# Optimization experiments

Measured on AMD Instinct MI355X. Metric: run time of the kernel, lower is better.

Reference implementation:

```python
import jax, jax.numpy as jnp
import numpy as np

B, MUL = 512, 64
DIMS = {0: 1, 1: 3, 2: 5}
PAIRS = [(0, 0), (0, 1), (0, 2), (1, 1), (1, 2), (2, 2)]  # l2 >= l1 (filter_symmetric)
LS_OUT = (0, 1, 2)


def _triples():
    for l1, l2 in PAIRS:
        for l3 in range(abs(l1 - l2), l1 + l2 + 1):
            if l3 in LS_OUT:
                yield (l1, l2, l3)


def setup_inputs() -> dict:
    key = jax.random.key(0)
    inp = {}
    for l in LS_OUT:
        key, k = jax.random.split(key)
        inp['x%d' % l] = jax.random.normal(k, (B, MUL, DIMS[l]), dtype=jnp.float32)
    for (l1, l2, l3) in _triples():
        key, k = jax.random.split(key)
        inp['w3j_%d_%d_%d' % (l1, l2, l3)] = jax.random.normal(
            k, (DIMS[l1], DIMS[l2], DIMS[l3]), dtype=jnp.float32) * 0.1
    return inp


def _forward(x, w):
    # ls_rule='full', channel_rule='full', filter_symmetric=True
    out = {l3: [] for l3 in LS_OUT}
    for l1, l2 in PAIRS:
        # outer product over channels and m-components: [B, i*j, 2l1+1, 2l2+1]
        op = jnp.einsum('bim,bjn->bijmn', x[l1], x[l2])
        b, i, j, m, n = op.shape
        op = op.reshape(b, i * j, m, n)
        for l3 in range(abs(l1 - l2), l1 + l2 + 1):
            if l3 in LS_OUT:
                # contract with Clebsch-Gordan / w3j coefficients
                out[l3].append(jnp.einsum('mnM,bimn->biM', w[(l1, l2, l3)], op))
    return tuple(jnp.concatenate(out[l3], axis=1) for l3 in LS_OUT)


def reference(x0, x1, x2,
              w3j_0_0_0, w3j_0_1_1, w3j_0_2_2,
              w3j_1_1_0, w3j_1_1_1, w3j_1_1_2,
              w3j_1_2_1, w3j_1_2_2,
              w3j_2_2_0, w3j_2_2_1, w3j_2_2_2):
    x = {0: x0, 1: x1, 2: x2}
    w = {(0, 0, 0): w3j_0_0_0, (0, 1, 1): w3j_0_1_1, (0, 2, 2): w3j_0_2_2,
         (1, 1, 0): w3j_1_1_0, (1, 1, 1): w3j_1_1_1, (1, 1, 2): w3j_1_1_2,
         (1, 2, 1): w3j_1_2_1, (1, 2, 2): w3j_1_2_2,
         (2, 2, 0): w3j_2_2_0, (2, 2, 1): w3j_2_2_1, (2, 2, 2): w3j_2_2_2}
    return _forward(x, w)
```

## Files before the change

kernel.cpp:

```cpp
#include <hip/hip_runtime.h>


#define OUT1_BASE (512 * 12288)
#define OUT2_BASE (OUT1_BASE + 512 * 49152)

template<int D1, int D2, int D3>
__device__ __forceinline__ void do_path(const float* __restrict__ w,
                                        const float* a, const float* bv,
                                        float* __restrict__ op)
{
    float wa[D2 * D3];
#pragma unroll
    for (int k = 0; k < D2 * D3; ++k) wa[k] = 0.f;
#pragma unroll
    for (int m = 0; m < D1; ++m) {
        const float am = a[m];
#pragma unroll
        for (int n = 0; n < D2; ++n)
#pragma unroll
            for (int M = 0; M < D3; ++M)
                wa[n * D3 + M] += w[(m * D2 + n) * D3 + M] * am;
    }

    float o[4 * D3];
#pragma unroll
    for (int k = 0; k < 4 * D3; ++k) o[k] = 0.f;
#pragma unroll
    for (int jj = 0; jj < 4; ++jj)
#pragma unroll
        for (int n = 0; n < D2; ++n) {
            const float bb = bv[jj * D2 + n];
#pragma unroll
            for (int M = 0; M < D3; ++M)
                o[jj * D3 + M] += wa[n * D3 + M] * bb;
        }

#pragma unroll
    for (int q = 0; q < D3; ++q) {
        float4 v;
        v.x = o[4 * q + 0]; v.y = o[4 * q + 1];
        v.z = o[4 * q + 2]; v.w = o[4 * q + 3];
        *(float4*)(op + 4 * q) = v;
    }
}

__global__ __launch_bounds__(256) void tp_kernel(
    const float* __restrict__ x0, const float* __restrict__ x1, const float* __restrict__ x2,
    const float* __restrict__ w000, const float* __restrict__ w011, const float* __restrict__ w022,
    const float* __restrict__ w110, const float* __restrict__ w111, const float* __restrict__ w112,
    const float* __restrict__ w121, const float* __restrict__ w122,
    const float* __restrict__ w220, const float* __restrict__ w221, const float* __restrict__ w222,
    float* __restrict__ out)
{
    const int b   = blockIdx.x >> 2;
    const int seg = blockIdx.x & 3;
    const int t   = threadIdx.x;
    const int c0  = seg * 1024 + t * 4;
    const int i   = c0 >> 6;
    const int j0  = c0 & 63;

    const float a0[1] = { x0[b * 64 + i] };
    float a1[3], a2[5];
#pragma unroll
    for (int m = 0; m < 3; ++m) a1[m] = x1[b * 192 + i * 3 + m];
#pragma unroll
    for (int m = 0; m < 5; ++m) a2[m] = x2[b * 320 + i * 5 + m];

    float b0v[4], b1v[12], b2v[20];
    {
        const float4 v = *(const float4*)(x0 + b * 64 + j0);
        b0v[0] = v.x; b0v[1] = v.y; b0v[2] = v.z; b0v[3] = v.w;
    }
#pragma unroll
    for (int k = 0; k < 3; ++k) {
        const float4 v = *(const float4*)(x1 + b * 192 + j0 * 3 + 4 * k);
        b1v[4 * k + 0] = v.x; b1v[4 * k + 1] = v.y;
        b1v[4 * k + 2] = v.z; b1v[4 * k + 3] = v.w;
    }
#pragma unroll
    for (int k = 0; k < 5; ++k) {
        const float4 v = *(const float4*)(x2 + b * 320 + j0 * 5 + 4 * k);
        b2v[4 * k + 0] = v.x; b2v[4 * k + 1] = v.y;
        b2v[4 * k + 2] = v.z; b2v[4 * k + 3] = v.w;
    }

    float* __restrict__ o0 = out + b * 12288;
    float* __restrict__ o1 = out + OUT1_BASE + b * 49152;
    float* __restrict__ o2 = out + OUT2_BASE + b * 81920;

    do_path<1, 1, 1>(w000, a0, b0v, o0 + 0 * 4096 + c0);

    do_path<1, 3, 3>(w011, a0, b1v, o1 + 0 * 12288 + c0 * 3);

    do_path<1, 5, 5>(w022, a0, b2v, o2 + 0 * 20480 + c0 * 5);

    do_path<3, 3, 1>(w110, a1, b1v, o0 + 1 * 4096 + c0);
    do_path<3, 3, 3>(w111, a1, b1v, o1 + 1 * 12288 + c0 * 3);
    do_path<3, 3, 5>(w112, a1, b1v, o2 + 1 * 20480 + c0 * 5);

    do_path<3, 5, 3>(w121, a1, b2v, o1 + 2 * 12288 + c0 * 3);
    do_path<3, 5, 5>(w122, a1, b2v, o2 + 2 * 20480 + c0 * 5);

    do_path<5, 5, 1>(w220, a2, b2v, o0 + 2 * 4096 + c0);
    do_path<5, 5, 3>(w221, a2, b2v, o1 + 3 * 12288 + c0 * 3);
    do_path<5, 5, 5>(w222, a2, b2v, o2 + 3 * 20480 + c0 * 5);
}

extern "C" void kernel_launch(void* const* d_in, const int* in_sizes, int n_in,
                              void* d_out, int out_size, void* d_ws, size_t ws_size,
                              hipStream_t stream) {
    const float* x0   = (const float*)d_in[0];
    const float* x1   = (const float*)d_in[1];
    const float* x2   = (const float*)d_in[2];
    const float* w000 = (const float*)d_in[3];
    const float* w011 = (const float*)d_in[4];
    const float* w022 = (const float*)d_in[5];
    const float* w110 = (const float*)d_in[6];
    const float* w111 = (const float*)d_in[7];
    const float* w112 = (const float*)d_in[8];
    const float* w121 = (const float*)d_in[9];
    const float* w122 = (const float*)d_in[10];
    const float* w220 = (const float*)d_in[11];
    const float* w221 = (const float*)d_in[12];
    const float* w222 = (const float*)d_in[13];
    float* outp = (float*)d_out;

    dim3 grid(512 * 4);
    dim3 block(256);
    tp_kernel<<<grid, block, 0, stream>>>(x0, x1, x2,
                                          w000, w011, w022, w110, w111, w112,
                                          w121, w122, w220, w221, w222, outp);
}
```

Measured before the change: 358.7 us.

## Stage l=1 and l=2 outputs through shared memory for coalesced stores

After: 320.9 us. -10.5%, faster.

```diff
diff --git a/kernel.cpp b/kernel.cpp
--- a/kernel.cpp
+++ b/kernel.cpp
@@ -5,9 +5,9 @@
 #define OUT2_BASE (OUT1_BASE + 512 * 49152)
 
 template<int D1, int D2, int D3>
-__device__ __forceinline__ void do_path(const float* __restrict__ w,
-                                        const float* a, const float* bv,
-                                        float* __restrict__ op)
+__device__ __forceinline__ void path_compute(const float* __restrict__ w,
+                                             const float* a, const float* bv,
+                                             float* __restrict__ o)
 {
     float wa[D2 * D3];
 #pragma unroll
@@ -21,8 +21,6 @@
             for (int M = 0; M < D3; ++M)
                 wa[n * D3 + M] += w[(m * D2 + n) * D3 + M] * am;
     }
-
-    float o[4 * D3];
 #pragma unroll
     for (int k = 0; k < 4 * D3; ++k) o[k] = 0.f;
 #pragma unroll
@@ -34,14 +32,27 @@
             for (int M = 0; M < D3; ++M)
                 o[jj * D3 + M] += wa[n * D3 + M] * bb;
         }
+}
 
+template<int D3>
+__device__ __forceinline__ void stage(float* __restrict__ s, int dwbase,
+                                      const float* __restrict__ o)
+{
 #pragma unroll
     for (int q = 0; q < D3; ++q) {
         float4 v;
         v.x = o[4 * q + 0]; v.y = o[4 * q + 1];
         v.z = o[4 * q + 2]; v.w = o[4 * q + 3];
-        *(float4*)(op + 4 * q) = v;
+        *(float4*)(s + dwbase + 4 * q) = v;
     }
+}
+
+__device__ __forceinline__ void store_f4(float* __restrict__ p,
+                                         const float* __restrict__ o)
+{
+    float4 v;
+    v.x = o[0]; v.y = o[1]; v.z = o[2]; v.w = o[3];
+    *(float4*)p = v;
 }
 
 __global__ __launch_bounds__(256) void tp_kernel(
@@ -52,6 +63,8 @@
     const float* __restrict__ w220, const float* __restrict__ w221, const float* __restrict__ w222,
     float* __restrict__ out)
 {
+    __shared__ __align__(16) float s_out[8192];
+
     const int b   = blockIdx.x >> 2;
     const int seg = blockIdx.x & 3;
     const int t   = threadIdx.x;
@@ -85,25 +98,52 @@
     }
 
     float* __restrict__ o0 = out + b * 12288;
-    float* __restrict__ o1 = out + OUT1_BASE + b * 49152;
-    float* __restrict__ o2 = out + OUT2_BASE + b * 81920;
+    const int o1base = OUT1_BASE + b * 49152 + seg * 3072;
+    const int o2base = OUT2_BASE + b * 81920 + seg * 5120;
 
-    do_path<1, 1, 1>(w000, a0, b0v, o0 + 0 * 4096 + c0);
+    float o[20];
 
-    do_path<1, 3, 3>(w011, a0, b1v, o1 + 0 * 12288 + c0 * 3);
+    {
+        float oo[4];
+#pragma unroll
+        for (int jj = 0; jj < 4; ++jj) oo[jj] = w000[0] * (a0[0] * b0v[jj]);
+        store_f4(o0 + c0, oo);
+    }
+    path_compute<1, 3, 3>(w011, a0, b1v, o);  stage<3>(s_out, t * 12, o);
+    path_compute<1, 5, 5>(w022, a0, b2v, o);  stage<5>(s_out, 3072 + t * 20, o);
 
-    do_path<1, 5, 5>(w022, a0, b2v, o2 + 0 * 20480 + c0 * 5);
+#pragma unroll
+    for (int r = 0; r < 4; ++r) {
+        __syncthreads();
+#pragma unroll
+        for (int kk = 0; kk < 8; ++kk) {
+            const int fi = kk * 256 + t;
+            float4 v = *(const float4*)(s_out + 4 * fi);
+            int dst;
+            if (fi < 768) dst = o1base + r * 12288 + 4 * fi;
+            else          dst = o2base + r * 20480 + 4 * (fi - 768);
+            *(float4*)(out + dst) = v;
+        }
+        if (r == 3) break;
+        __syncthreads();
 
-    do_path<3, 3, 1>(w110, a1, b1v, o0 + 1 * 4096 + c0);
-    do_path<3, 3, 3>(w111, a1, b1v, o1 + 1 * 12288 + c0 * 3);
-    do_path<3, 3, 5>(w112, a1, b1v, o2 + 1 * 20480 + c0 * 5);
-
-    do_path<3, 5, 3>(w121, a1, b2v, o1 + 2 * 12288 + c0 * 3);
-    do_path<3, 5, 5>(w122, a1, b2v, o2 + 2 * 20480 + c0 * 5);
-
-    do_path<5, 5, 1>(w220, a2, b2v, o0 + 2 * 4096 + c0);
-    do_path<5, 5, 3>(w221, a2, b2v, o1 + 3 * 12288 + c0 * 3);
-    do_path<5, 5, 5>(w222, a2, b2v, o2 + 3 * 20480 + c0 * 5);
+        if (r == 0) {
+            float oo[4];
+            path_compute<3, 3, 1>(w110, a1, b1v, oo);
+            store_f4(o0 + 4096 + c0, oo);
+            path_compute<3, 3, 3>(w111, a1, b1v, o);  stage<3>(s_out, t * 12, o);
+            path_compute<3, 3, 5>(w112, a1, b1v, o);  stage<5>(s_out, 3072 + t * 20, o);
+        } else if (r == 1) {
+            path_compute<3, 5, 3>(w121, a1, b2v, o);  stage<3>(s_out, t * 12, o);
+            path_compute<3, 5, 5>(w122, a1, b2v, o);  stage<5>(s_out, 3072 + t * 20, o);
+        } else {
+            float oo[4];
+            path_compute<5, 5, 1>(w220, a2, b2v, oo);
+            store_f4(o0 + 8192 + c0, oo);
+            path_compute<5, 5, 3>(w221, a2, b2v, o);  stage<3>(s_out, t * 12, o);
+            path_compute<5, 5, 5>(w222, a2, b2v, o);  stage<5>(s_out, 3072 + t * 20, o);
+        }
+    }
 }
 
 extern "C" void kernel_launch(void* const* d_in, const int* in_sizes, int n_in,
```

## Stage l=1/l=2 outputs through per-wave LDS for fully coalesced stores

Applied to the files above, without the earlier changes.

Result: faster. 322.7 us (-10.0%).

```diff
diff --git a/kernel.cpp b/kernel.cpp
--- a/kernel.cpp
+++ b/kernel.cpp
@@ -4,10 +4,15 @@
 #define OUT1_BASE (512 * 12288)
 #define OUT2_BASE (OUT1_BASE + 512 * 49152)
 
+#define LDS_FENCE() do {                                  \
+    asm volatile("s_waitcnt lgkmcnt(0)" ::: "memory");    \
+    __builtin_amdgcn_sched_barrier(0);                    \
+} while (0)
+
 template<int D1, int D2, int D3>
-__device__ __forceinline__ void do_path(const float* __restrict__ w,
-                                        const float* a, const float* bv,
-                                        float* __restrict__ op)
+__device__ __forceinline__ void path_compute(const float* __restrict__ w,
+                                             const float* a, const float* bv,
+                                             float* o)
 {
     float wa[D2 * D3];
 #pragma unroll
@@ -21,8 +26,6 @@
             for (int M = 0; M < D3; ++M)
                 wa[n * D3 + M] += w[(m * D2 + n) * D3 + M] * am;
     }
-
-    float o[4 * D3];
 #pragma unroll
     for (int k = 0; k < 4 * D3; ++k) o[k] = 0.f;
 #pragma unroll
@@ -34,15 +37,42 @@
             for (int M = 0; M < D3; ++M)
                 o[jj * D3 + M] += wa[n * D3 + M] * bb;
         }
+}
 
-#pragma unroll
-    for (int q = 0; q < D3; ++q) {
-        float4 v;
-        v.x = o[4 * q + 0]; v.y = o[4 * q + 1];
-        v.z = o[4 * q + 2]; v.w = o[4 * q + 3];
-        *(float4*)(op + 4 * q) = v;
-    }
-}
+#define STAGE3(optr) do {                                          \
+    _Pragma("unroll")                                              \
+    for (int q = 0; q < 3; ++q) {                                  \
+        float4 v;                                                  \
+        v.x = (optr)[4*q+0]; v.y = (optr)[4*q+1];                  \
+        v.z = (optr)[4*q+2]; v.w = (optr)[4*q+3];                  \
+        *(float4*)(sw + ln * 12 + 4 * q) = v;                      \
+    }                                                              \
+} while (0)
+
+#define STAGE5(optr) do {                                          \
+    _Pragma("unroll")                                              \
+    for (int q = 0; q < 5; ++q) {                                  \
+        float4 v;                                                  \
+        v.x = (optr)[4*q+0]; v.y = (optr)[4*q+1];                  \
+        v.z = (optr)[4*q+2]; v.w = (optr)[4*q+3];                  \
+        *(float4*)(sw + 768 + ln * 20 + 4 * q) = v;                \
+    }                                                              \
+} while (0)
+
+#define FLUSH_ROUND(r) do {                                        \
+    _Pragma("unroll")                                              \
+    for (int q = 0; q < 3; ++q) {                                  \
+        const int fo = 4 * (ln + 64 * q);                          \
+        float4 v = *(const float4*)(sw + fo);                      \
+        *(float4*)(out + o1base + (r) * 12288 + fo) = v;           \
+    }                                                              \
+    _Pragma("unroll")                                              \
+    for (int q = 0; q < 5; ++q) {                                  \
+        const int fo = 4 * (ln + 64 * q);                          \
+        float4 v = *(const float4*)(sw + 768 + fo);                \
+        *(float4*)(out + o2base + (r) * 20480 + fo) = v;           \
+    }                                                              \
+} while (0)
 
 __global__ __launch_bounds__(256) void tp_kernel(
     const float* __restrict__ x0, const float* __restrict__ x1, const float* __restrict__ x2,
@@ -50,14 +80,20 @@
     const float* __restrict__ w110, const float* __restrict__ w111, const float* __restrict__ w112,
     const float* __restrict__ w121, const float* __restrict__ w122,
     const float* __restrict__ w220, const float* __restrict__ w221, const float* __restrict__ w222,
-    float* __restrict__ out)
+    float* out)
 {
+    __shared__ __align__(16) float s_out[8192];
+
     const int b   = blockIdx.x >> 2;
     const int seg = blockIdx.x & 3;
     const int t   = threadIdx.x;
+    const int wv  = t >> 6;
+    const int ln  = t & 63;
     const int c0  = seg * 1024 + t * 4;
     const int i   = c0 >> 6;
     const int j0  = c0 & 63;
+
+    float* sw = s_out + wv * 2048;
 
     const float a0[1] = { x0[b * 64 + i] };
     float a1[3], a2[5];
@@ -84,26 +120,50 @@
         b2v[4 * k + 2] = v.z; b2v[4 * k + 3] = v.w;
     }
 
-    float* __restrict__ o0 = out + b * 12288;
-    float* __restrict__ o1 = out + OUT1_BASE + b * 49152;
-    float* __restrict__ o2 = out + OUT2_BASE + b * 81920;
+    float* o0 = out + b * 12288;
+    const int o1base = OUT1_BASE + b * 49152 + seg * 3072 + wv * 768;
+    const int o2base = OUT2_BASE + b * 81920 + seg * 5120 + wv * 1280;
 
-    do_path<1, 1, 1>(w000, a0, b0v, o0 + 0 * 4096 + c0);
+    float o[20], oo[4];
 
-    do_path<1, 3, 3>(w011, a0, b1v, o1 + 0 * 12288 + c0 * 3);
+#pragma unroll
+    for (int jj = 0; jj < 4; ++jj) oo[jj] = w000[0] * (a0[0] * b0v[jj]);
+    {
+        float4 v; v.x = oo[0]; v.y = oo[1]; v.z = oo[2]; v.w = oo[3];
+        *(float4*)(o0 + c0) = v;
+    }
+    path_compute<1, 3, 3>(w011, a0, b1v, o);  STAGE3(o);
+    path_compute<1, 5, 5>(w022, a0, b2v, o);  STAGE5(o);
+    LDS_FENCE();
+    FLUSH_ROUND(0);
+    LDS_FENCE();
 
-    do_path<1, 5, 5>(w022, a0, b2v, o2 + 0 * 20480 + c0 * 5);
+    path_compute<3, 3, 1>(w110, a1, b1v, oo);
+    {
+        float4 v; v.x = oo[0]; v.y = oo[1]; v.z = oo[2]; v.w = oo[3];
+        *(float4*)(o0 + 4096 + c0) = v;
+    }
+    path_compute<3, 3, 3>(w111, a1, b1v, o);  STAGE3(o);
+    path_compute<3, 3, 5>(w112, a1, b1v, o);  STAGE5(o);
+    LDS_FENCE();
+    FLUSH_ROUND(1);
+    LDS_FENCE();
 
-    do_path<3, 3, 1>(w110, a1, b1v, o0 + 1 * 4096 + c0);
-    do_path<3, 3, 3>(w111, a1, b1v, o1 + 1 * 12288 + c0 * 3);
-    do_path<3, 3, 5>(w112, a1, b1v, o2 + 1 * 20480 + c0 * 5);
+    path_compute<3, 5, 3>(w121, a1, b2v, o);  STAGE3(o);
+    path_compute<3, 5, 5>(w122, a1, b2v, o);  STAGE5(o);
+    LDS_FENCE();
+    FLUSH_ROUND(2);
+    LDS_FENCE();
 
-    do_path<3, 5, 3>(w121, a1, b2v, o1 + 2 * 12288 + c0 * 3);
-    do_path<3, 5, 5>(w122, a1, b2v, o2 + 2 * 20480 + c0 * 5);
-
-    do_path<5, 5, 1>(w220, a2, b2v, o0 + 2 * 4096 + c0);
-    do_path<5, 5, 3>(w221, a2, b2v, o1 + 3 * 12288 + c0 * 3);
-    do_path<5, 5, 5>(w222, a2, b2v, o2 + 3 * 20480 + c0 * 5);
+    path_compute<5, 5, 1>(w220, a2, b2v, oo);
+    {
+        float4 v; v.x = oo[0]; v.y = oo[1]; v.z = oo[2]; v.w = oo[3];
+        *(float4*)(o0 + 8192 + c0) = v;
+    }
+    path_compute<5, 5, 3>(w221, a2, b2v, o);  STAGE3(o);
+    path_compute<5, 5, 5>(w222, a2, b2v, o);  STAGE5(o);
+    LDS_FENCE();
+    FLUSH_ROUND(3);
 }
 
 extern "C" void kernel_launch(void* const* d_in, const int* in_sizes, int n_in,
```
